# Optimization experiments

Measured on AMD Instinct MI355X. Metric: run time of the kernel, lower is better.

The kernel has to match this reference:

```python
import jax, jax.numpy as jnp
import numpy as np

EMBED_DIM = 1024
NUM_HEADS = 16
HEAD_DIM = EMBED_DIM // NUM_HEADS  # used only for the softmax scale


def setup_inputs() -> dict:
    key = jax.random.key(0)
    k_x, k_wqkv, k_bqkv, k_wo, k_bo = jax.random.split(key, 5)
    bound_qkv = 1.0 / np.sqrt(EMBED_DIM)
    return {
        "x": jax.random.normal(k_x, (4, 2048, EMBED_DIM), dtype=jnp.float32),
        "W_qkv": jax.random.uniform(k_wqkv, (EMBED_DIM, 3 * EMBED_DIM), jnp.float32, -bound_qkv, bound_qkv),
        "b_qkv": jax.random.uniform(k_bqkv, (3 * EMBED_DIM,), jnp.float32, -bound_qkv, bound_qkv),
        "W_out": jax.random.uniform(k_wo, (EMBED_DIM, EMBED_DIM), jnp.float32, -bound_qkv, bound_qkv),
        "b_out": jax.random.uniform(k_bo, (EMBED_DIM,), jnp.float32, -bound_qkv, bound_qkv),
    }


def reference(x, W_qkv, b_qkv, W_out, b_out):
    # fused QKV projection: [B,S,3E]
    qkv = jnp.einsum("bse,ef->bsf", x, W_qkv) + b_qkv
    q, k, v = jnp.split(qkv, 3, axis=-1)  # each [B,S,E]
    scale = 1.0 / jnp.sqrt(jnp.float32(HEAD_DIM))
    # NOTE: no head reshape — attention over full embed_dim, scale uses head_dim
    scores = jnp.einsum("bqe,bke->bqk", q, k) * scale  # [B,S,S]
    attn = jax.nn.softmax(scores, axis=-1)
    context = jnp.einsum("bqk,bke->bqe", attn, v)  # [B,S,E]
    return jnp.einsum("bse,ef->bsf", context, W_out) + b_out
```

## Files before the change

kernel.cpp:

```cpp
#include <hip/hip_runtime.h>

typedef unsigned short u16;
typedef __bf16   bf16x8 __attribute__((ext_vector_type(8)));
typedef float    f32x4  __attribute__((ext_vector_type(4)));
typedef unsigned short u16x4 __attribute__((ext_vector_type(4)));

__device__ inline float bf2f(u16 u) { return __uint_as_float(((unsigned int)u) << 16); }
__device__ inline u16 f2bf(float f) {
    unsigned int u = __float_as_uint(f);
    u += 0x7FFF + ((u >> 16) & 1);
    return (u16)(u >> 16);
}

__device__ inline void gl2lds16(const u16* g, u16* l) {
    __builtin_amdgcn_global_load_lds(
        (const __attribute__((address_space(1))) void*)g,
        (__attribute__((address_space(3))) void*)l, 16, 0, 0);
}

__global__ void sniff_dtype(const u16* __restrict__ x, int* __restrict__ flag) {
    const int lane = threadIdx.x;
    const unsigned idx = lane * 131072u + 65536u;
    const u16 u = x[idx];
    const int e = (u >> 7) & 0xFF;
    const unsigned long long b = __ballot(e >= 100 && e <= 140);
    if (lane == 0) flag[0] = (__popcll(b) >= 48) ? 0 : 1;
}

__global__ __launch_bounds__(256)
void zero_f32(float* __restrict__ p) {
    p[blockIdx.x * 256 + threadIdx.x] = 0.0f;
}

__global__ __launch_bounds__(256)
void convx(const void* __restrict__ in, u16* __restrict__ out, const int* __restrict__ flagp) {
    const long i = ((long)blockIdx.x * 256 + threadIdx.x) * 4;
    if (*flagp) {
        f32x4 v = *(const f32x4*)((const float*)in + i);
        u16x4 o; o[0] = f2bf(v[0]); o[1] = f2bf(v[1]); o[2] = f2bf(v[2]); o[3] = f2bf(v[3]);
        *(u16x4*)(out + i) = o;
    } else {
        *(u16x4*)(out + i) = *(const u16x4*)((const u16*)in + i);
    }
}

__global__ __launch_bounds__(256)
void conv_biases(const void* __restrict__ b1, const void* __restrict__ b2,
                 u16* __restrict__ o1, u16* __restrict__ o2,
                 const int* __restrict__ flagp) {
    const int i = blockIdx.x * 256 + threadIdx.x;
    const int f = *flagp;
    if (i < 3072) o1[i] = f ? f2bf(((const float*)b1)[i]) : ((const u16*)b1)[i];
    else { const int j = i - 3072;
           o2[j] = f ? f2bf(((const float*)b2)[j]) : ((const u16*)b2)[j]; }
}

template <int GM, int GN, int WM, int WN, int EPI, int OUT_MODE, bool HAS_BIAS>
__global__ __launch_bounds__(256, 4)
void gemm_t(const u16* __restrict__ A, const u16* __restrict__ Bt,
            void* __restrict__ Cv, const u16* __restrict__ bias,
            int K, long lda, long ldb, long ldc,
            long aBatch, long bBatch, long cBatch, float scale,
            const int* __restrict__ flagp, float* __restrict__ sums)
{
    constexpr int BM = GM * WM * 16;
    constexpr int BN = GN * WN * 16;
    constexpr int IA = BM / 32;
    constexpr int IB = BN / 32;
    __shared__ __align__(16) u16 As[BM * 64];
    __shared__ __align__(16) u16 Bs[BN * 64];

    const int outF32 = (OUT_MODE == 2) ? *flagp : OUT_MODE;

    const int tid  = threadIdx.x;
    const int lane = tid & 63;
    const int wave = tid >> 6;
    const long m0 = (long)blockIdx.y * BM;
    const long n0 = (long)blockIdx.x * BN;
    const long bz = blockIdx.z;

    const int sr  = tid >> 3;
    const int qg0 = (tid & 7) ^ (sr & 7);
    const u16* pa[IA];
    const u16* pb[IB];
    u16* la[IA];
    u16* lb[IB];
#pragma unroll
    for (int i = 0; i < IA; ++i) {
        pa[i] = A + bz * aBatch + (m0 + i * 32 + sr) * lda + qg0 * 8;
        la[i] = As + (i * 256 + wave * 64) * 8;
    }
#pragma unroll
    for (int i = 0; i < IB; ++i) {
        pb[i] = Bt + bz * bBatch + (n0 + i * 32 + sr) * ldb + qg0 * 8;
        lb[i] = Bs + (i * 256 + wave * 64) * 8;
    }

    const int wm = (wave / GN) * (WM * 16);
    const int wn = (wave % GN) * (WN * 16);
    const int lr = lane & 15;
    const int hk = lane >> 4;

    int aoff[WM][2], boff[WN][2];
#pragma unroll
    for (int i = 0; i < WM; ++i) {
        const int row = wm + i * 16 + lr, r7 = row & 7;
        aoff[i][0] = row * 64 + ((hk     ^ r7) * 8);
        aoff[i][1] = row * 64 + (((4+hk) ^ r7) * 8);
    }
#pragma unroll
    for (int j = 0; j < WN; ++j) {
        const int row = wn + j * 16 + lr, r7 = row & 7;
        boff[j][0] = row * 64 + ((hk     ^ r7) * 8);
        boff[j][1] = row * 64 + (((4+hk) ^ r7) * 8);
    }

    f32x4 acc[WM][WN] = {};

    for (int kt = 0; kt < K; kt += 64) {
#pragma unroll
        for (int i = 0; i < IA; ++i) { gl2lds16(pa[i], la[i]); pa[i] += 64; }
#pragma unroll
        for (int i = 0; i < IB; ++i) { gl2lds16(pb[i], lb[i]); pb[i] += 64; }
        __syncthreads();

#pragma unroll
        for (int ks = 0; ks < 2; ++ks) {
            bf16x8 af[WM], bf[WN];
#pragma unroll
            for (int i = 0; i < WM; ++i) af[i] = *(const bf16x8*)&As[aoff[i][ks]];
#pragma unroll
            for (int j = 0; j < WN; ++j) bf[j] = *(const bf16x8*)&Bs[boff[j][ks]];
#pragma unroll
            for (int i = 0; i < WM; ++i)
#pragma unroll
                for (int j = 0; j < WN; ++j)
                    acc[i][j] = __builtin_amdgcn_mfma_f32_16x16x32_bf16(af[i], bf[j], acc[i][j], 0, 0, 0);
        }
        __syncthreads();
    }

    if (EPI == 1) {
#pragma unroll
        for (int i = 0; i < WM; ++i) {
#pragma unroll
            for (int r = 0; r < 4; ++r) {
                const long row = m0 + wm + i*16 + hk*4 + r;
                float s = 0.0f;
#pragma unroll
                for (int j = 0; j < WN; ++j) {
                    const long c = n0 + wn + j*16 + lr;
                    const float e = __expf(acc[i][j][r] * scale);
                    ((u16*)Cv)[bz * cBatch + row * ldc + c] = f2bf(e);
                    s += e;
                }
                s += __shfl_xor(s, 1); s += __shfl_xor(s, 2);
                s += __shfl_xor(s, 4); s += __shfl_xor(s, 8);
                if (lr == 0) atomicAdd(&sums[bz * 2048 + row], s);
            }
        }
    } else {
        float inv[WM][4];
        if (EPI == 2) {
#pragma unroll
            for (int i = 0; i < WM; ++i)
#pragma unroll
                for (int r = 0; r < 4; ++r)
                    inv[i][r] = 1.0f / sums[bz * 2048 + m0 + wm + i*16 + hk*4 + r];
        }
#pragma unroll
        for (int j = 0; j < WN; ++j) {
            const long c = n0 + wn + j*16 + lr;
            const float bj = HAS_BIAS ? bf2f(bias[c]) : 0.0f;
#pragma unroll
            for (int i = 0; i < WM; ++i) {
                const long rbase = m0 + wm + i*16 + hk * 4;
#pragma unroll
                for (int r = 0; r < 4; ++r) {
                    float v = (EPI == 2) ? acc[i][j][r] * inv[i][r]
                                         : acc[i][j][r] * scale + bj;
                    const long ci = bz * cBatch + (rbase + r) * ldc + c;
                    if (outF32) ((float*)Cv)[ci] = v;
                    else        ((u16*)Cv)[ci]   = f2bf(v);
                }
            }
        }
    }
}

__global__ __launch_bounds__(256)
void transpose_any(const void* __restrict__ in, u16* __restrict__ out,
                   long inStride, long outStride, const int* __restrict__ flagp)
{
    __shared__ u16 t[32][36];
    const int isF32 = *flagp;
    const int tid = threadIdx.x;
    const long r0 = (long)blockIdx.y * 32;
    const long c0 = (long)blockIdx.x * 32;
    const int r  = tid >> 3;
    const int c4 = (tid & 7) * 4;
    const long base = (r0 + r) * inStride + c0 + c4;
    u16x4 v;
    if (isF32) {
        f32x4 f = *(const f32x4*)((const float*)in + base);
        v[0] = f2bf(f[0]); v[1] = f2bf(f[1]); v[2] = f2bf(f[2]); v[3] = f2bf(f[3]);
    } else {
        v = *(const u16x4*)((const u16*)in + base);
    }
    t[r][c4 + 0] = v[0]; t[r][c4 + 1] = v[1]; t[r][c4 + 2] = v[2]; t[r][c4 + 3] = v[3];
    __syncthreads();
    u16x4 o;
    o[0] = t[c4 + 0][r]; o[1] = t[c4 + 1][r]; o[2] = t[c4 + 2][r]; o[3] = t[c4 + 3][r];
    *(u16x4*)&out[(c0 + r) * outStride + r0 + c4] = o;
}

__global__ __launch_bounds__(256)
void transpose_bf16(const u16* __restrict__ in, u16* __restrict__ out,
                    long inStride, long outStride, long inBatch, long outBatch)
{
    __shared__ u16 t[32][36];
    const int tid = threadIdx.x;
    const long r0 = (long)blockIdx.y * 32;
    const long c0 = (long)blockIdx.x * 32;
    in  += (long)blockIdx.z * inBatch;
    out += (long)blockIdx.z * outBatch;
    const int r  = tid >> 3;
    const int c4 = (tid & 7) * 4;
    u16x4 v = *(const u16x4*)&in[(r0 + r) * inStride + c0 + c4];
    t[r][c4 + 0] = v[0]; t[r][c4 + 1] = v[1]; t[r][c4 + 2] = v[2]; t[r][c4 + 3] = v[3];
    __syncthreads();
    u16x4 o;
    o[0] = t[c4 + 0][r]; o[1] = t[c4 + 1][r]; o[2] = t[c4 + 2][r]; o[3] = t[c4 + 3][r];
    *(u16x4*)&out[(c0 + r) * outStride + r0 + c4] = o;
}

extern "C" void kernel_launch(void* const* d_in, const int* in_sizes, int n_in,
                              void* d_out, int out_size, void* d_ws, size_t ws_size,
                              hipStream_t stream)
{
    const void* x    = d_in[0];
    const void* Wqkv = d_in[1];
    const void* bqkv = d_in[2];
    const void* Wout = d_in[3];
    const void* bout = d_in[4];
    char* ws = (char*)d_ws;

    u16*   xbf   = (u16*)(ws);
    u16*   WqkvT = (u16*)(ws + 16777216);
    u16*   P     = (u16*)(ws);
    u16*   QKV   = (u16*)(ws + 33554432);
    u16*   VT    = (u16*)(ws + 83886080);
    u16*   CTX   = (u16*)(ws + 100663296);
    u16*   WoutT = (u16*)(ws + 117440512);
    u16*   bqkvc = (u16*)(ws + 119537664);
    u16*   boutc = (u16*)(ws + 119543808);
    int*   flag  = (int*)(ws + 119545856);
    float* sums  = (float*)(ws + 119549952);

    dim3 blk(256);

    sniff_dtype<<<1, 64, 0, stream>>>((const u16*)x, flag);
    zero_f32<<<32, blk, 0, stream>>>(sums);
    convx<<<8192, blk, 0, stream>>>(x, xbf, flag);
    conv_biases<<<16, blk, 0, stream>>>(bqkv, bout, bqkvc, boutc, flag);
    transpose_any<<<dim3(96, 32), blk, 0, stream>>>(Wqkv, WqkvT, 3072L, 1024L, flag);
    transpose_any<<<dim3(32, 32), blk, 0, stream>>>(Wout, WoutT, 1024L, 1024L, flag);

    gemm_t<2, 2, 4, 4, 0, 0, true><<<dim3(24, 64, 1), blk, 0, stream>>>(
        xbf, WqkvT, QKV, bqkvc, 1024, 1024L, 1024L, 3072L,
        0L, 0L, 0L, 1.0f, nullptr, nullptr);

    transpose_bf16<<<dim3(32, 64, 4), blk, 0, stream>>>(
        QKV + 2048, VT, 3072L, 2048L, 2048L * 3072L, 1024L * 2048L);

    gemm_t<2, 2, 4, 4, 1, 0, false><<<dim3(16, 16, 4), blk, 0, stream>>>(
        QKV, QKV + 1024, P, nullptr, 1024, 3072L, 3072L, 2048L,
        2048L * 3072L, 2048L * 3072L, 2048L * 2048L, 0.125f, nullptr, sums);

    gemm_t<4, 1, 2, 4, 2, 0, false><<<dim3(16, 16, 4), blk, 0, stream>>>(
        P, VT, CTX, nullptr, 2048, 2048L, 2048L, 1024L,
        2048L * 2048L, 1024L * 2048L, 2048L * 1024L, 1.0f, nullptr, sums);

    gemm_t<4, 1, 2, 4, 0, 2, true><<<dim3(16, 64, 1), blk, 0, stream>>>(
        CTX, WoutT, d_out, boutc, 1024, 1024L, 1024L, 1024L,
        0L, 0L, 0L, 1.0f, flag, nullptr);
}
```

Baseline: 295.5 us.

## Reassociate output projection into V and fuse launch-overhead kernels

New measurement: 276.3 us. 6.5% less time.

```diff
diff --git a/kernel.cpp b/kernel.cpp
--- a/kernel.cpp
+++ b/kernel.cpp
@@ -18,41 +18,72 @@
         (__attribute__((address_space(3))) void*)l, 16, 0, 0);
 }
 
-__global__ void sniff_dtype(const u16* __restrict__ x, int* __restrict__ flag) {
-    const int lane = threadIdx.x;
-    const unsigned idx = lane * 131072u + 65536u;
-    const u16 u = x[idx];
-    const int e = (u >> 7) & 0xFF;
-    const unsigned long long b = __ballot(e >= 100 && e <= 140);
-    if (lane == 0) flag[0] = (__popcll(b) >= 48) ? 0 : 1;
-}
-
 __global__ __launch_bounds__(256)
-void zero_f32(float* __restrict__ p) {
-    p[blockIdx.x * 256 + threadIdx.x] = 0.0f;
+void sniff_zero(const u16* __restrict__ x, int* __restrict__ flag,
+                float* __restrict__ sums) {
+    sums[blockIdx.x * 256 + threadIdx.x] = 0.0f;
+    if (blockIdx.x == 0 && threadIdx.x < 64) {
+        const int lane = threadIdx.x;
+        const unsigned idx = lane * 131072u + 65536u;
+        const u16 u = x[idx];
+        const int e = (u >> 7) & 0xFF;
+        const unsigned long long b = __ballot(e >= 100 && e <= 140);
+        if (lane == 0) flag[0] = (__popcll(b) >= 48) ? 0 : 1;
+    }
 }
 
 __global__ __launch_bounds__(256)
-void convx(const void* __restrict__ in, u16* __restrict__ out, const int* __restrict__ flagp) {
-    const long i = ((long)blockIdx.x * 256 + threadIdx.x) * 4;
-    if (*flagp) {
-        f32x4 v = *(const f32x4*)((const float*)in + i);
-        u16x4 o; o[0] = f2bf(v[0]); o[1] = f2bf(v[1]); o[2] = f2bf(v[2]); o[3] = f2bf(v[3]);
-        *(u16x4*)(out + i) = o;
+void convx_biases(const void* __restrict__ x, u16* __restrict__ xbf,
+                  const void* __restrict__ b1, const void* __restrict__ b2,
+                  u16* __restrict__ o1, u16* __restrict__ o2,
+                  const int* __restrict__ flagp) {
+    const int f = *flagp;
+    if (blockIdx.x < 8192) {
+        const long i = ((long)blockIdx.x * 256 + threadIdx.x) * 4;
+        if (f) {
+            f32x4 v = *(const f32x4*)((const float*)x + i);
+            u16x4 o; o[0] = f2bf(v[0]); o[1] = f2bf(v[1]); o[2] = f2bf(v[2]); o[3] = f2bf(v[3]);
+            *(u16x4*)(xbf + i) = o;
+        } else {
+            *(u16x4*)(xbf + i) = *(const u16x4*)((const u16*)x + i);
+        }
     } else {
-        *(u16x4*)(out + i) = *(const u16x4*)((const u16*)in + i);
+        const int i = (blockIdx.x - 8192) * 256 + threadIdx.x;
+        if (i < 3072) o1[i] = f ? f2bf(((const float*)b1)[i]) : ((const u16*)b1)[i];
+        else { const int j = i - 3072;
+               o2[j] = f ? f2bf(((const float*)b2)[j]) : ((const u16*)b2)[j]; }
     }
 }
 
 __global__ __launch_bounds__(256)
-void conv_biases(const void* __restrict__ b1, const void* __restrict__ b2,
-                 u16* __restrict__ o1, u16* __restrict__ o2,
-                 const int* __restrict__ flagp) {
-    const int i = blockIdx.x * 256 + threadIdx.x;
-    const int f = *flagp;
-    if (i < 3072) o1[i] = f ? f2bf(((const float*)b1)[i]) : ((const u16*)b1)[i];
-    else { const int j = i - 3072;
-           o2[j] = f ? f2bf(((const float*)b2)[j]) : ((const u16*)b2)[j]; }
+void transpose_w(const void* __restrict__ Wqkv, u16* __restrict__ WqkvT,
+                 const void* __restrict__ Wout, u16* __restrict__ WoutT,
+                 const int* __restrict__ flagp)
+{
+    const void* in; u16* out; long inStride, outStride;
+    if (blockIdx.z == 0) { in = Wqkv; out = WqkvT; inStride = 3072; outStride = 1024; }
+    else { if (blockIdx.x >= 32) return;
+           in = Wout; out = WoutT; inStride = 1024; outStride = 1024; }
+    __shared__ u16 t[32][36];
+    const int isF32 = *flagp;
+    const int tid = threadIdx.x;
+    const long r0 = (long)blockIdx.y * 32;
+    const long c0 = (long)blockIdx.x * 32;
+    const int r  = tid >> 3;
+    const int c4 = (tid & 7) * 4;
+    const long base = (r0 + r) * inStride + c0 + c4;
+    u16x4 v;
+    if (isF32) {
+        f32x4 f = *(const f32x4*)((const float*)in + base);
+        v[0] = f2bf(f[0]); v[1] = f2bf(f[1]); v[2] = f2bf(f[2]); v[3] = f2bf(f[3]);
+    } else {
+        v = *(const u16x4*)((const u16*)in + base);
+    }
+    t[r][c4 + 0] = v[0]; t[r][c4 + 1] = v[1]; t[r][c4 + 2] = v[2]; t[r][c4 + 3] = v[3];
+    __syncthreads();
+    u16x4 o;
+    o[0] = t[c4 + 0][r]; o[1] = t[c4 + 1][r]; o[2] = t[c4 + 2][r]; o[3] = t[c4 + 3][r];
+    *(u16x4*)&out[(c0 + r) * outStride + r0 + c4] = o;
 }
 
 template <int GM, int GN, int WM, int WN, int EPI, int OUT_MODE, bool HAS_BIAS>
@@ -177,7 +208,7 @@
                 const long rbase = m0 + wm + i*16 + hk * 4;
 #pragma unroll
                 for (int r = 0; r < 4; ++r) {
-                    float v = (EPI == 2) ? acc[i][j][r] * inv[i][r]
+                    float v = (EPI == 2) ? acc[i][j][r] * inv[i][r] + bj
                                          : acc[i][j][r] * scale + bj;
                     const long ci = bz * cBatch + (rbase + r) * ldc + c;
                     if (outF32) ((float*)Cv)[ci] = v;
@@ -186,52 +217,6 @@
             }
         }
     }
-}
-
-__global__ __launch_bounds__(256)
-void transpose_any(const void* __restrict__ in, u16* __restrict__ out,
-                   long inStride, long outStride, const int* __restrict__ flagp)
-{
-    __shared__ u16 t[32][36];
-    const int isF32 = *flagp;
-    const int tid = threadIdx.x;
-    const long r0 = (long)blockIdx.y * 32;
-    const long c0 = (long)blockIdx.x * 32;
-    const int r  = tid >> 3;
-    const int c4 = (tid & 7) * 4;
-    const long base = (r0 + r) * inStride + c0 + c4;
-    u16x4 v;
-    if (isF32) {
-        f32x4 f = *(const f32x4*)((const float*)in + base);
-        v[0] = f2bf(f[0]); v[1] = f2bf(f[1]); v[2] = f2bf(f[2]); v[3] = f2bf(f[3]);
-    } else {
-        v = *(const u16x4*)((const u16*)in + base);
-    }
-    t[r][c4 + 0] = v[0]; t[r][c4 + 1] = v[1]; t[r][c4 + 2] = v[2]; t[r][c4 + 3] = v[3];
-    __syncthreads();
-    u16x4 o;
-    o[0] = t[c4 + 0][r]; o[1] = t[c4 + 1][r]; o[2] = t[c4 + 2][r]; o[3] = t[c4 + 3][r];
-    *(u16x4*)&out[(c0 + r) * outStride + r0 + c4] = o;
-}
-
-__global__ __launch_bounds__(256)
-void transpose_bf16(const u16* __restrict__ in, u16* __restrict__ out,
-                    long inStride, long outStride, long inBatch, long outBatch)
-{
-    __shared__ u16 t[32][36];
-    const int tid = threadIdx.x;
-    const long r0 = (long)blockIdx.y * 32;
-    const long c0 = (long)blockIdx.x * 32;
-    in  += (long)blockIdx.z * inBatch;
-    out += (long)blockIdx.z * outBatch;
-    const int r  = tid >> 3;
-    const int c4 = (tid & 7) * 4;
-    u16x4 v = *(const u16x4*)&in[(r0 + r) * inStride + c0 + c4];
-    t[r][c4 + 0] = v[0]; t[r][c4 + 1] = v[1]; t[r][c4 + 2] = v[2]; t[r][c4 + 3] = v[3];
-    __syncthreads();
-    u16x4 o;
-    o[0] = t[c4 + 0][r]; o[1] = t[c4 + 1][r]; o[2] = t[c4 + 2][r]; o[3] = t[c4 + 3][r];
-    *(u16x4*)&out[(c0 + r) * outStride + r0 + c4] = o;
 }
 
 extern "C" void kernel_launch(void* const* d_in, const int* in_sizes, int n_in,
@@ -249,39 +234,32 @@
     u16*   WqkvT = (u16*)(ws + 16777216);
     u16*   P     = (u16*)(ws);
     u16*   QKV   = (u16*)(ws + 33554432);
-    u16*   VT    = (u16*)(ws + 83886080);
-    u16*   CTX   = (u16*)(ws + 100663296);
-    u16*   WoutT = (u16*)(ws + 117440512);
-    u16*   bqkvc = (u16*)(ws + 119537664);
-    u16*   boutc = (u16*)(ws + 119543808);
-    int*   flag  = (int*)(ws + 119545856);
-    float* sums  = (float*)(ws + 119549952);
+    u16*   VWT   = (u16*)(ws + 83886080);
+    u16*   WoutT = (u16*)(ws + 100663296);
+    u16*   bqkvc = (u16*)(ws + 102760448);
+    u16*   boutc = (u16*)(ws + 102766592);
+    int*   flag  = (int*)(ws + 102768640);
+    float* sums  = (float*)(ws + 102772736);
 
     dim3 blk(256);
 
-    sniff_dtype<<<1, 64, 0, stream>>>((const u16*)x, flag);
-    zero_f32<<<32, blk, 0, stream>>>(sums);
-    convx<<<8192, blk, 0, stream>>>(x, xbf, flag);
-    conv_biases<<<16, blk, 0, stream>>>(bqkv, bout, bqkvc, boutc, flag);
-    transpose_any<<<dim3(96, 32), blk, 0, stream>>>(Wqkv, WqkvT, 3072L, 1024L, flag);
-    transpose_any<<<dim3(32, 32), blk, 0, stream>>>(Wout, WoutT, 1024L, 1024L, flag);
+    sniff_zero<<<32, blk, 0, stream>>>((const u16*)x, flag, sums);
+    convx_biases<<<8208, blk, 0, stream>>>(x, xbf, bqkv, bout, bqkvc, boutc, flag);
+    transpose_w<<<dim3(96, 32, 2), blk, 0, stream>>>(Wqkv, WqkvT, Wout, WoutT, flag);
 
     gemm_t<2, 2, 4, 4, 0, 0, true><<<dim3(24, 64, 1), blk, 0, stream>>>(
         xbf, WqkvT, QKV, bqkvc, 1024, 1024L, 1024L, 3072L,
         0L, 0L, 0L, 1.0f, nullptr, nullptr);
 
-    transpose_bf16<<<dim3(32, 64, 4), blk, 0, stream>>>(
-        QKV + 2048, VT, 3072L, 2048L, 2048L * 3072L, 1024L * 2048L);
+    gemm_t<2, 2, 4, 4, 0, 0, false><<<dim3(16, 8, 4), blk, 0, stream>>>(
+        WoutT, QKV + 2048, VWT, nullptr, 1024, 1024L, 3072L, 2048L,
+        0L, 2048L * 3072L, 1024L * 2048L, 1.0f, nullptr, nullptr);
 
     gemm_t<2, 2, 4, 4, 1, 0, false><<<dim3(16, 16, 4), blk, 0, stream>>>(
         QKV, QKV + 1024, P, nullptr, 1024, 3072L, 3072L, 2048L,
         2048L * 3072L, 2048L * 3072L, 2048L * 2048L, 0.125f, nullptr, sums);
 
-    gemm_t<4, 1, 2, 4, 2, 0, false><<<dim3(16, 16, 4), blk, 0, stream>>>(
-        P, VT, CTX, nullptr, 2048, 2048L, 2048L, 1024L,
-        2048L * 2048L, 1024L * 2048L, 2048L * 1024L, 1.0f, nullptr, sums);
-
-    gemm_t<4, 1, 2, 4, 0, 2, true><<<dim3(16, 64, 1), blk, 0, stream>>>(
-        CTX, WoutT, d_out, boutc, 1024, 1024L, 1024L, 1024L,
-        0L, 0L, 0L, 1.0f, flag, nullptr);
-}
+    gemm_t<2, 2, 4, 4, 2, 2, true><<<dim3(8, 16, 4), blk, 0, stream>>>(
+        P, VWT, d_out, boutc, 2048, 2048L, 2048L, 1024L,
+        2048L * 2048L, 1024L * 2048L, 2048L * 1024L, 1.0f, flag, sums);
+}
```
